# Kernel tuning notes

Measured on AMD Instinct MI355X. Metric: run time of the kernel, lower is better.

## Reference

```python
import jax, jax.numpy as jnp
import numpy as np
import math

NUM_HEADS = 16
THETA = 10000.0


def _rope(x):
    # x: (B, L, H, hd); interleaved-pair rotary embedding
    B, L, H, hd = x.shape
    inv_freq = 1.0 / (THETA ** (jnp.arange(0, hd, 2, dtype=jnp.float32) / hd))  # (hd/2,)
    ang = jnp.arange(L, dtype=jnp.float32)[:, None] * inv_freq[None, :]         # (L, hd/2)
    cos = jnp.cos(ang)[None, :, None, :].astype(x.dtype)
    sin = jnp.sin(ang)[None, :, None, :].astype(x.dtype)
    x1 = x[..., 0::2]
    x2 = x[..., 1::2]
    r1 = x1 * cos - x2 * sin
    r2 = x1 * sin + x2 * cos
    return jnp.stack([r1, r2], axis=-1).reshape(x.shape)


def setup_inputs() -> dict:
    key = jax.random.key(0)
    ks = jax.random.split(key, 5)
    B, L, D = 4, 2048, 1024
    x = jax.random.normal(ks[0], (B, L, D), dtype=jnp.float32)
    scale = 0.02
    wq = jax.random.normal(ks[1], (D, D), dtype=jnp.float32) * scale
    wk = jax.random.normal(ks[2], (D, D), dtype=jnp.float32) * scale
    wv = jax.random.normal(ks[3], (D, D), dtype=jnp.float32) * scale
    wo = jax.random.normal(ks[4], (D, D), dtype=jnp.float32) * scale
    return {"x": x, "wq": wq, "wk": wk, "wv": wv, "wo": wo}


def reference(x, wq, wk, wv, wo):
    B, L, D = x.shape
    H = NUM_HEADS
    hd = D // H
    q = (x @ wq).reshape(B, L, H, hd)
    k = (x @ wk).reshape(B, L, H, hd)
    v = (x @ wv).reshape(B, L, H, hd)
    q = _rope(q)
    k = _rope(k)
    # (B, H, L, hd)
    q = q.transpose(0, 2, 1, 3)
    k = k.transpose(0, 2, 1, 3)
    v = v.transpose(0, 2, 1, 3)
    # default-mask path of forward(): float 0/1 mask over key positions added to scores
    mask = (jnp.sum(x, axis=-1) != 0).astype(x.dtype)[:, None, None, :]  # (B,1,1,L)
    scale_factor = 1.0 / math.sqrt(hd)
    scores = jnp.einsum("bhld,bhsd->bhls", q, k) * scale_factor + mask
    attn = jax.nn.softmax(scores, axis=-1)
    out = jnp.einsum("bhls,bhsd->bhld", attn, v)          # (B,H,L,hd)
    out = out.transpose(0, 2, 1, 3).reshape(B, L, D)
    return out @ wo
```

## Files before the change

### kernel.cpp

```cpp
#include <hip/hip_runtime.h>

typedef __bf16 bf16_t;
typedef bf16_t bf16x8 __attribute__((ext_vector_type(8)));
typedef bf16_t bf16x4 __attribute__((ext_vector_type(4)));
typedef float f32x4 __attribute__((ext_vector_type(4)));

__device__ __forceinline__ ushort f2bu(float f) {
  unsigned u = __float_as_uint(f);
  unsigned r = (u + 0x7fffu + ((u >> 16) & 1u)) >> 16;
  return (ushort)r;
}
__device__ __forceinline__ float b2f(ushort u) {
  return __uint_as_float(((unsigned)u) << 16);
}

typedef const __attribute__((address_space(1))) unsigned int* gas_ptr;
typedef __attribute__((address_space(3))) unsigned int* las_ptr;
__device__ __forceinline__ void g2l16(const void* g, void* l) {
  __builtin_amdgcn_global_load_lds((gas_ptr)g, (las_ptr)l, 16, 0, 0);
}

__global__ __launch_bounds__(256) void pack_x(const float* __restrict__ x,
                                              ushort* __restrict__ xb,
                                              float* __restrict__ maskv) {
  int row = blockIdx.x;
  int tid = threadIdx.x;
  const float4 v = ((const float4*)(x + (size_t)row * 1024))[tid];
  ushort4 o;
  o.x = f2bu(v.x); o.y = f2bu(v.y); o.z = f2bu(v.z); o.w = f2bu(v.w);
  ((ushort4*)(xb + (size_t)row * 1024))[tid] = o;
  float s = v.x + v.y + v.z + v.w;
#pragma unroll
  for (int m = 1; m < 64; m <<= 1) s += __shfl_xor(s, m);
  __shared__ float wsum[4];
  if ((tid & 63) == 0) wsum[tid >> 6] = s;
  __syncthreads();
  if (tid == 0)
    maskv[row] = ((wsum[0] + wsum[1] + wsum[2] + wsum[3]) != 0.f)
                     ? 1.4426950408889634f : 0.f;
}

__global__ __launch_bounds__(1024) void pack_w(const float* __restrict__ w,
                                               ushort* __restrict__ wt) {
  __shared__ float t[32][33];
  int n0 = blockIdx.x * 32, k0 = blockIdx.y * 32;
  int tx = threadIdx.x, ty = threadIdx.y;
  t[ty][tx] = w[(size_t)(k0 + ty) * 1024 + n0 + tx];
  __syncthreads();
  wt[(size_t)(n0 + ty) * 1024 + k0 + tx] = f2bu(t[tx][ty]);
}

__global__ __launch_bounds__(256) void gemm_bf16(const ushort* __restrict__ A,
                                                 const ushort* __restrict__ BT,
                                                 void* __restrict__ Cv,
                                                 int M, int N, int K, int mode) {
  __shared__ ushort lA[128 * 64];
  __shared__ ushort lB[128 * 64];
  const int tid = threadIdx.x;
  const int wave = tid >> 6, lane = tid & 63;
  const int lr = lane & 15, lk = lane >> 4;
  const int bm = blockIdx.x * 128, bn = blockIdx.y * 128;
  const int wr = (wave >> 1) * 64, wc = (wave & 1) * 64;
  f32x4 acc[4][4] = {};
  for (int kt = 0; kt < K; kt += 64) {
#pragma unroll
    for (int t = 0; t < 4; ++t) {
      int e = (t * 256 + tid) * 8;
      int row = e >> 6, col = e & 63;
      g2l16(A + (size_t)(bm + row) * K + kt + col, lA + e);
      g2l16(BT + (size_t)(bn + row) * K + kt + col, lB + e);
    }
    __syncthreads();
#pragma unroll
    for (int ks = 0; ks < 2; ++ks) {
      bf16x8 af[4], bfr[4];
#pragma unroll
      for (int i = 0; i < 4; ++i)
        af[i] = *(const bf16x8*)(lA + (wr + i * 16 + lr) * 64 + ks * 32 + lk * 8);
#pragma unroll
      for (int j = 0; j < 4; ++j)
        bfr[j] = *(const bf16x8*)(lB + (wc + j * 16 + lr) * 64 + ks * 32 + lk * 8);
#pragma unroll
      for (int i = 0; i < 4; ++i)
#pragma unroll
        for (int j = 0; j < 4; ++j)
          acc[i][j] = __builtin_amdgcn_mfma_f32_16x16x32_bf16(af[i], bfr[j],
                                                              acc[i][j], 0, 0, 0);
    }
    __syncthreads();
  }
#pragma unroll
  for (int i = 0; i < 4; ++i)
#pragma unroll
    for (int j = 0; j < 4; ++j)
#pragma unroll
      for (int r = 0; r < 4; ++r) {
        int m = bm + wr + i * 16 + lk * 4 + r;
        int n = bn + wc + j * 16 + lr;
        float v = acc[i][j][r];
        if (mode == 2) {
          ((float*)Cv)[(size_t)m * N + n] = v;
        } else {
          int b = m >> 11, l = m & 2047;
          int h = n >> 6, d = n & 63;
          size_t addr;
          if (mode == 0) addr = (((size_t)b * 16 + h) * 2048 + l) * 64 + d;
          else           addr = (((size_t)b * 16 + h) * 64 + d) * 2048 + l;
          ((ushort*)Cv)[addr] = f2bu(v);
        }
      }
}

__global__ __launch_bounds__(256) void rope_k(ushort* __restrict__ Qb,
                                              ushort* __restrict__ Kb) {
  const size_t P1 = (size_t)64 * 2048 * 32;
  size_t id = (size_t)blockIdx.x * 256 + threadIdx.x;
  ushort* base = Qb;
  size_t rr = id;
  if (id >= P1) { base = Kb; rr = id - P1; }
  int i = (int)(rr & 31);
  int l = (int)((rr >> 5) & 2047);
  size_t bh = rr >> 16;
  size_t addr = (bh * 2048 + (size_t)l) * 64 + 2 * i;
  unsigned p = *(const unsigned*)(base + addr);
  float x1 = b2f((ushort)(p & 0xffffu));
  float x2 = b2f((ushort)(p >> 16));
  const float c = 0.41524101186092029f;
  float inv = exp2f(-c * (float)i);
  float ang = (float)l * inv;
  float sv, cv;
  sincosf(ang, &sv, &cv);
  float r1 = x1 * cv - x2 * sv;
  float r2 = x1 * sv + x2 * cv;
  unsigned o = (unsigned)f2bu(r1) | ((unsigned)f2bu(r2) << 16);
  *(unsigned*)(base + addr) = o;
}

__global__ __launch_bounds__(256) void attn_k(const ushort* __restrict__ Qb,
                                              const ushort* __restrict__ Kb,
                                              const ushort* __restrict__ VTb,
                                              const float* __restrict__ maskv,
                                              ushort* __restrict__ Ob) {
  __shared__ ushort lK[128 * 64];
  __shared__ ushort lV[64 * 128];
  __shared__ ushort lP[4][32 * 128];
  const int tid = threadIdx.x;
  const int wave = tid >> 6, lane = tid & 63;
  const int lr = lane & 15, lk = lane >> 4;
  const int bh = blockIdx.y;
  const int b = bh >> 4, h = bh & 15;
  const int q0 = blockIdx.x * 128 + wave * 32;
  const ushort* qp = Qb + (size_t)bh * 2048 * 64;
  const ushort* kp = Kb + (size_t)bh * 2048 * 64;
  const ushort* vp = VTb + (size_t)bh * 64 * 2048;
  const float SCL = 0.18033688011112042f;

  bf16x8 qfr[2][2];
#pragma unroll
  for (int qf = 0; qf < 2; ++qf)
#pragma unroll
    for (int ks = 0; ks < 2; ++ks)
      qfr[qf][ks] = *(const bf16x8*)(qp + (size_t)(q0 + qf * 16 + lr) * 64 +
                                     ks * 32 + lk * 8);

  float m2[2] = {-1e30f, -1e30f}, ls[2] = {0.f, 0.f};
  f32x4 oacc[2][4] = {};

  const int krow = tid >> 3;
  const int kslot = (tid & 7) ^ (krow & 7);
  const int vrow = tid >> 4;
  const int vslot = (tid & 15) ^ (vrow & 15);

  for (int kt = 0; kt < 16; ++kt) {
#pragma unroll
    for (int t = 0; t < 4; ++t) {
      g2l16(kp + (size_t)(kt * 128 + t * 32 + krow) * 64 + kslot * 8,
            lK + (t * 256 + tid) * 8);
      g2l16(vp + (size_t)(t * 16 + vrow) * 2048 + kt * 128 + vslot * 8,
            lV + (t * 256 + tid) * 8);
    }
    __syncthreads();

    f32x4 sacc[8][2] = {};
#pragma unroll
    for (int ks = 0; ks < 2; ++ks)
#pragma unroll
      for (int kf = 0; kf < 8; ++kf) {
        bf16x8 kfr = *(const bf16x8*)(lK + (kf * 16 + lr) * 64 +
                                      ((ks * 32 + lk * 8) ^ ((lr & 7) << 3)));
#pragma unroll
        for (int qf = 0; qf < 2; ++qf)
          sacc[kf][qf] = __builtin_amdgcn_mfma_f32_16x16x32_bf16(
              kfr, qfr[qf][ks], sacc[kf][qf], 0, 0, 0);
      }

    const f32x4* mrow = (const f32x4*)(maskv + (size_t)b * 2048 + kt * 128);
#pragma unroll
    for (int kf = 0; kf < 8; ++kf) {
      f32x4 mk = mrow[kf * 4 + lk];
#pragma unroll
      for (int qf = 0; qf < 2; ++qf) sacc[kf][qf] = sacc[kf][qf] * SCL + mk;
    }

    float corr[2];
#pragma unroll
    for (int qf = 0; qf < 2; ++qf) {
      float mx = -1e30f;
#pragma unroll
      for (int kf = 0; kf < 8; ++kf)
#pragma unroll
        for (int r = 0; r < 4; ++r) mx = fmaxf(mx, sacc[kf][qf][r]);
      mx = fmaxf(mx, __shfl_xor(mx, 16));
      mx = fmaxf(mx, __shfl_xor(mx, 32));
      float mnew = fmaxf(m2[qf], mx);
      corr[qf] = __builtin_amdgcn_exp2f(m2[qf] - mnew);
      m2[qf] = mnew;
      float ps = 0.f;
#pragma unroll
      for (int kf = 0; kf < 8; ++kf) {
        f32x4 p;
#pragma unroll
        for (int r = 0; r < 4; ++r)
          p[r] = __builtin_amdgcn_exp2f(sacc[kf][qf][r] - mnew);
        ps += (p[0] + p[1]) + (p[2] + p[3]);
        bf16x4 pb;
#pragma unroll
        for (int r = 0; r < 4; ++r) pb[r] = (bf16_t)p[r];
        int slot = (kf * 2 + (lk >> 1)) ^ lr;
        *(bf16x4*)&lP[wave][(qf * 16 + lr) * 128 + slot * 8 + (lk & 1) * 4] = pb;
      }
      ps += __shfl_xor(ps, 16);
      ps += __shfl_xor(ps, 32);
      ls[qf] = ls[qf] * corr[qf] + ps;
    }

#pragma unroll
    for (int mf = 0; mf < 2; ++mf)
#pragma unroll
      for (int r = 0; r < 4; ++r) {
        float c = __shfl(corr[mf], lk * 4 + r);
#pragma unroll
        for (int df = 0; df < 4; ++df) oacc[mf][df][r] *= c;
      }

#pragma unroll
    for (int ks2 = 0; ks2 < 4; ++ks2) {
      bf16x8 pf[2];
#pragma unroll
      for (int mf = 0; mf < 2; ++mf)
        pf[mf] = *(const bf16x8*)(&lP[wave][(mf * 16 + lr) * 128 +
                                            (((ks2 * 4 + lk) ^ lr) << 3)]);
#pragma unroll
      for (int df = 0; df < 4; ++df) {
        bf16x8 vf = *(const bf16x8*)(lV + (df * 16 + lr) * 128 +
                                     ((ks2 * 32 + lk * 8) ^ (lr << 3)));
#pragma unroll
        for (int mf = 0; mf < 2; ++mf)
          oacc[mf][df] = __builtin_amdgcn_mfma_f32_16x16x32_bf16(
              pf[mf], vf, oacc[mf][df], 0, 0, 0);
      }
    }
    __syncthreads();
  }

#pragma unroll
  for (int mf = 0; mf < 2; ++mf) {
    float inv[4];
#pragma unroll
    for (int r = 0; r < 4; ++r) inv[r] = 1.f / __shfl(ls[mf], lk * 4 + r);
#pragma unroll
    for (int df = 0; df < 4; ++df)
#pragma unroll
      for (int r = 0; r < 4; ++r) {
        int l = q0 + mf * 16 + lk * 4 + r;
        int d = df * 16 + lr;
        Ob[((size_t)b * 2048 + l) * 1024 + h * 64 + d] =
            f2bu(oacc[mf][df][r] * inv[r]);
      }
  }
}

extern "C" void kernel_launch(void* const* d_in, const int* in_sizes, int n_in,
                              void* d_out, int out_size, void* d_ws, size_t ws_size,
                              hipStream_t stream) {
  const float* x  = (const float*)d_in[0];
  const float* wq = (const float*)d_in[1];
  const float* wk = (const float*)d_in[2];
  const float* wv = (const float*)d_in[3];
  const float* wo = (const float*)d_in[4];
  float* out = (float*)d_out;
  char* ws = (char*)d_ws;
  const size_t MB = 1024 * 1024;
  ushort* xb   = (ushort*)(ws);
  ushort* ao   = (ushort*)(ws);
  ushort* wqT  = (ushort*)(ws + 16 * MB);
  ushort* wkT  = (ushort*)(ws + 18 * MB);
  ushort* wvT  = (ushort*)(ws + 20 * MB);
  ushort* woT  = (ushort*)(ws + 22 * MB);
  ushort* qb   = (ushort*)(ws + 24 * MB);
  ushort* kb   = (ushort*)(ws + 40 * MB);
  ushort* vtb  = (ushort*)(ws + 56 * MB);
  float* maskv = (float*)(ws + 72 * MB);

  pack_x<<<8192, 256, 0, stream>>>(x, xb, maskv);
  dim3 tb(32, 32);
  pack_w<<<dim3(32, 32), tb, 0, stream>>>(wq, wqT);
  pack_w<<<dim3(32, 32), tb, 0, stream>>>(wk, wkT);
  pack_w<<<dim3(32, 32), tb, 0, stream>>>(wv, wvT);
  pack_w<<<dim3(32, 32), tb, 0, stream>>>(wo, woT);
  gemm_bf16<<<dim3(64, 8), 256, 0, stream>>>(xb, wqT, qb, 8192, 1024, 1024, 0);
  gemm_bf16<<<dim3(64, 8), 256, 0, stream>>>(xb, wkT, kb, 8192, 1024, 1024, 0);
  gemm_bf16<<<dim3(64, 8), 256, 0, stream>>>(xb, wvT, vtb, 8192, 1024, 1024, 1);
  rope_k<<<32768, 256, 0, stream>>>(qb, kb);
  attn_k<<<dim3(16, 64), 256, 0, stream>>>(qb, kb, vtb, maskv, ao);
  gemm_bf16<<<dim3(64, 8), 256, 0, stream>>>(ao, woT, out, 8192, 1024, 1024, 2);
}
```

Measured before the change: 411.4 us.

## Rewrite attention with 32x32 MFMA, register-held P, and double-buffered K/V

```diff
diff --git a/kernel.cpp b/kernel.cpp
--- a/kernel.cpp
+++ b/kernel.cpp
@@ -3,7 +3,10 @@
 typedef __bf16 bf16_t;
 typedef bf16_t bf16x8 __attribute__((ext_vector_type(8)));
 typedef bf16_t bf16x4 __attribute__((ext_vector_type(4)));
+typedef bf16_t bf16x2 __attribute__((ext_vector_type(2)));
 typedef float f32x4 __attribute__((ext_vector_type(4)));
+typedef float f32x16 __attribute__((ext_vector_type(16)));
+typedef unsigned int uint32x4 __attribute__((ext_vector_type(4)));
 
 __device__ __forceinline__ ushort f2bu(float f) {
   unsigned u = __float_as_uint(f);
@@ -136,148 +139,146 @@
   *(unsigned*)(base + addr) = o;
 }
 
-__global__ __launch_bounds__(256) void attn_k(const ushort* __restrict__ Qb,
-                                              const ushort* __restrict__ Kb,
-                                              const ushort* __restrict__ VTb,
-                                              const float* __restrict__ maskv,
-                                              ushort* __restrict__ Ob) {
-  __shared__ ushort lK[128 * 64];
-  __shared__ ushort lV[64 * 128];
-  __shared__ ushort lP[4][32 * 128];
+__global__ __launch_bounds__(512, 4) void attn_k(const ushort* __restrict__ Qb,
+                                                 const ushort* __restrict__ Kb,
+                                                 const ushort* __restrict__ VTb,
+                                                 const float* __restrict__ maskv,
+                                                 ushort* __restrict__ Ob) {
+  __shared__ ushort lK[2][4096];
+  __shared__ ushort lV[2][4096];
   const int tid = threadIdx.x;
-  const int wave = tid >> 6, lane = tid & 63;
-  const int lr = lane & 15, lk = lane >> 4;
-  const int bh = blockIdx.y;
-  const int b = bh >> 4, h = bh & 15;
-  const int q0 = blockIdx.x * 128 + wave * 32;
+  const int wid = tid >> 6, lane = tid & 63;
+  const int q = lane & 31, hi = lane >> 5;
+  int f = blockIdx.x;
+  int swz = (f & 7) * 64 + (f >> 3);
+  int qb_i = swz & 7, bh = swz >> 3;
+  int b = bh >> 4, h = bh & 15;
+  const int q0w = qb_i * 256 + wid * 32;
   const ushort* qp = Qb + (size_t)bh * 2048 * 64;
   const ushort* kp = Kb + (size_t)bh * 2048 * 64;
   const ushort* vp = VTb + (size_t)bh * 64 * 2048;
   const float SCL = 0.18033688011112042f;
 
-  bf16x8 qfr[2][2];
-#pragma unroll
-  for (int qf = 0; qf < 2; ++qf)
-#pragma unroll
-    for (int ks = 0; ks < 2; ++ks)
-      qfr[qf][ks] = *(const bf16x8*)(qp + (size_t)(q0 + qf * 16 + lr) * 64 +
-                                     ks * 32 + lk * 8);
-
-  float m2[2] = {-1e30f, -1e30f}, ls[2] = {0.f, 0.f};
-  f32x4 oacc[2][4] = {};
-
-  const int krow = tid >> 3;
-  const int kslot = (tid & 7) ^ (krow & 7);
-  const int vrow = tid >> 4;
-  const int vslot = (tid & 15) ^ (vrow & 15);
-
-  for (int kt = 0; kt < 16; ++kt) {
-#pragma unroll
-    for (int t = 0; t < 4; ++t) {
-      g2l16(kp + (size_t)(kt * 128 + t * 32 + krow) * 64 + kslot * 8,
-            lK + (t * 256 + tid) * 8);
-      g2l16(vp + (size_t)(t * 16 + vrow) * 2048 + kt * 128 + vslot * 8,
-            lV + (t * 256 + tid) * 8);
+  bf16x8 qfr[4];
+#pragma unroll
+  for (int s = 0; s < 4; ++s)
+    qfr[s] = *(const bf16x8*)(qp + (size_t)(q0w + q) * 64 + s * 16 + hi * 8);
+
+  f32x16 oacc[2] = {};
+  float m2 = -1e30f, ls = 0.f;
+
+  const int sr = tid >> 3;
+  const int ss = (tid & 7) ^ (sr & 7);
+  const ushort* kg = kp + sr * 64 + ss * 8;
+  const ushort* vg = vp + (size_t)sr * 2048 + ss * 8;
+  int roff[4];
+#pragma unroll
+  for (int j = 0; j < 4; ++j)
+    roff[j] = q * 128 + (((2 * j + hi) ^ (q & 7)) << 4);
+
+  g2l16(kg, (char*)lK + tid * 16);
+  g2l16(vg, (char*)lV + tid * 16);
+  __syncthreads();
+
+  int cur = 0;
+  for (int kt = 0; kt < 32; ++kt) {
+    if (kt < 31) {
+      g2l16(kg + (kt + 1) * 4096, (char*)lK + (cur ^ 1) * 8192 + tid * 16);
+      g2l16(vg + (kt + 1) * 64,   (char*)lV + (cur ^ 1) * 8192 + tid * 16);
+    }
+    const char* bK = (const char*)lK + cur * 8192;
+    f32x16 sacc[2] = {};
+#pragma unroll
+    for (int kb2 = 0; kb2 < 2; ++kb2)
+#pragma unroll
+      for (int s = 0; s < 4; ++s) {
+        bf16x8 kfr = *(const bf16x8*)(bK + kb2 * 4096 + roff[s]);
+        sacc[kb2] = __builtin_amdgcn_mfma_f32_32x32x16_bf16(kfr, qfr[s],
+                                                            sacc[kb2], 0, 0, 0);
+      }
+    const float* mbase = maskv + (size_t)b * 2048 + kt * 64;
+#pragma unroll
+    for (int kb2 = 0; kb2 < 2; ++kb2)
+#pragma unroll
+      for (int g = 0; g < 4; ++g) {
+        f32x4 mv = *(const f32x4*)(mbase + kb2 * 32 + g * 8 + 4 * hi);
+#pragma unroll
+        for (int e = 0; e < 4; ++e)
+          sacc[kb2][4 * g + e] = sacc[kb2][4 * g + e] * SCL + mv[e];
+      }
+    float mx = -1e30f;
+#pragma unroll
+    for (int r = 0; r < 16; ++r) mx = fmaxf(mx, fmaxf(sacc[0][r], sacc[1][r]));
+    mx = fmaxf(mx, __shfl_xor(mx, 32));
+    float mnew = fmaxf(m2, mx);
+    float corr = __builtin_amdgcn_exp2f(m2 - mnew);
+    m2 = mnew;
+    float ps = 0.f;
+#pragma unroll
+    for (int kb2 = 0; kb2 < 2; ++kb2)
+#pragma unroll
+      for (int r = 0; r < 16; ++r) {
+        float p = __builtin_amdgcn_exp2f(sacc[kb2][r] - mnew);
+        sacc[kb2][r] = p;
+        ps += p;
+      }
+    ps += __shfl_xor(ps, 32);
+    ls = ls * corr + ps;
+#pragma unroll
+    for (int d2 = 0; d2 < 2; ++d2)
+#pragma unroll
+      for (int r = 0; r < 16; ++r) oacc[d2][r] *= corr;
+
+    const char* bV = (const char*)lV + cur * 8192;
+#pragma unroll
+    for (int kb2 = 0; kb2 < 2; ++kb2) {
+      unsigned w[8];
+#pragma unroll
+      for (int j = 0; j < 8; ++j) {
+        bf16x2 t2;
+        t2[0] = (bf16_t)sacc[kb2][2 * j];
+        t2[1] = (bf16_t)sacc[kb2][2 * j + 1];
+        w[j] = __builtin_bit_cast(unsigned, t2);
+      }
+#pragma unroll
+      for (int sg = 0; sg < 2; ++sg) {
+        unsigned X0 = (unsigned)__shfl_xor((int)w[4 * sg + 0], 32);
+        unsigned X1 = (unsigned)__shfl_xor((int)w[4 * sg + 1], 32);
+        unsigned X2 = (unsigned)__shfl_xor((int)w[4 * sg + 2], 32);
+        unsigned X3 = (unsigned)__shfl_xor((int)w[4 * sg + 3], 32);
+        uint32x4 fw;
+        fw[0] = hi ? X2 : w[4 * sg + 0];
+        fw[1] = hi ? X3 : w[4 * sg + 1];
+        fw[2] = hi ? w[4 * sg + 2] : X0;
+        fw[3] = hi ? w[4 * sg + 3] : X1;
+        bf16x8 pfr = __builtin_bit_cast(bf16x8, fw);
+        int tau = kb2 * 2 + sg;
+#pragma unroll
+        for (int d2 = 0; d2 < 2; ++d2) {
+          bf16x8 vfr = *(const bf16x8*)(bV + d2 * 4096 + roff[tau]);
+          oacc[d2] = __builtin_amdgcn_mfma_f32_32x32x16_bf16(vfr, pfr,
+                                                             oacc[d2], 0, 0, 0);
+        }
+      }
     }
     __syncthreads();
-
-    f32x4 sacc[8][2] = {};
-#pragma unroll
-    for (int ks = 0; ks < 2; ++ks)
-#pragma unroll
-      for (int kf = 0; kf < 8; ++kf) {
-        bf16x8 kfr = *(const bf16x8*)(lK + (kf * 16 + lr) * 64 +
-                                      ((ks * 32 + lk * 8) ^ ((lr & 7) << 3)));
-#pragma unroll
-        for (int qf = 0; qf < 2; ++qf)
-          sacc[kf][qf] = __builtin_amdgcn_mfma_f32_16x16x32_bf16(
-              kfr, qfr[qf][ks], sacc[kf][qf], 0, 0, 0);
-      }
-
-    const f32x4* mrow = (const f32x4*)(maskv + (size_t)b * 2048 + kt * 128);
-#pragma unroll
-    for (int kf = 0; kf < 8; ++kf) {
-      f32x4 mk = mrow[kf * 4 + lk];
-#pragma unroll
-      for (int qf = 0; qf < 2; ++qf) sacc[kf][qf] = sacc[kf][qf] * SCL + mk;
-    }
-
-    float corr[2];
-#pragma unroll
-    for (int qf = 0; qf < 2; ++qf) {
-      float mx = -1e30f;
-#pragma unroll
-      for (int kf = 0; kf < 8; ++kf)
-#pragma unroll
-        for (int r = 0; r < 4; ++r) mx = fmaxf(mx, sacc[kf][qf][r]);
-      mx = fmaxf(mx, __shfl_xor(mx, 16));
-      mx = fmaxf(mx, __shfl_xor(mx, 32));
-      float mnew = fmaxf(m2[qf], mx);
-      corr[qf] = __builtin_amdgcn_exp2f(m2[qf] - mnew);
-      m2[qf] = mnew;
-      float ps = 0.f;
-#pragma unroll
-      for (int kf = 0; kf < 8; ++kf) {
-        f32x4 p;
-#pragma unroll
-        for (int r = 0; r < 4; ++r)
-          p[r] = __builtin_amdgcn_exp2f(sacc[kf][qf][r] - mnew);
-        ps += (p[0] + p[1]) + (p[2] + p[3]);
-        bf16x4 pb;
-#pragma unroll
-        for (int r = 0; r < 4; ++r) pb[r] = (bf16_t)p[r];
-        int slot = (kf * 2 + (lk >> 1)) ^ lr;
-        *(bf16x4*)&lP[wave][(qf * 16 + lr) * 128 + slot * 8 + (lk & 1) * 4] = pb;
-      }
-      ps += __shfl_xor(ps, 16);
-      ps += __shfl_xor(ps, 32);
-      ls[qf] = ls[qf] * corr[qf] + ps;
-    }
-
-#pragma unroll
-    for (int mf = 0; mf < 2; ++mf)
-#pragma unroll
-      for (int r = 0; r < 4; ++r) {
-        float c = __shfl(corr[mf], lk * 4 + r);
-#pragma unroll
-        for (int df = 0; df < 4; ++df) oacc[mf][df][r] *= c;
-      }
-
-#pragma unroll
-    for (int ks2 = 0; ks2 < 4; ++ks2) {
-      bf16x8 pf[2];
-#pragma unroll
-      for (int mf = 0; mf < 2; ++mf)
-        pf[mf] = *(const bf16x8*)(&lP[wave][(mf * 16 + lr) * 128 +
-                                            (((ks2 * 4 + lk) ^ lr) << 3)]);
-#pragma unroll
-      for (int df = 0; df < 4; ++df) {
-        bf16x8 vf = *(const bf16x8*)(lV + (df * 16 + lr) * 128 +
-                                     ((ks2 * 32 + lk * 8) ^ (lr << 3)));
-#pragma unroll
-        for (int mf = 0; mf < 2; ++mf)
-          oacc[mf][df] = __builtin_amdgcn_mfma_f32_16x16x32_bf16(
-              pf[mf], vf, oacc[mf][df], 0, 0, 0);
-      }
-    }
-    __syncthreads();
+    cur ^= 1;
   }
 
-#pragma unroll
-  for (int mf = 0; mf < 2; ++mf) {
-    float inv[4];
-#pragma unroll
-    for (int r = 0; r < 4; ++r) inv[r] = 1.f / __shfl(ls[mf], lk * 4 + r);
-#pragma unroll
-    for (int df = 0; df < 4; ++df)
-#pragma unroll
-      for (int r = 0; r < 4; ++r) {
-        int l = q0 + mf * 16 + lk * 4 + r;
-        int d = df * 16 + lr;
-        Ob[((size_t)b * 2048 + l) * 1024 + h * 64 + d] =
-            f2bu(oacc[mf][df][r] * inv[r]);
-      }
-  }
+  float inv = 1.f / ls;
+  const int l = q0w + q;
+#pragma unroll
+  for (int d2 = 0; d2 < 2; ++d2)
+#pragma unroll
+    for (int g = 0; g < 4; ++g) {
+      ushort4 o;
+      o.x = f2bu(oacc[d2][4 * g + 0] * inv);
+      o.y = f2bu(oacc[d2][4 * g + 1] * inv);
+      o.z = f2bu(oacc[d2][4 * g + 2] * inv);
+      o.w = f2bu(oacc[d2][4 * g + 3] * inv);
+      int dcol = d2 * 32 + g * 8 + 4 * hi;
+      *(ushort4*)(Ob + ((size_t)b * 2048 + l) * 1024 + h * 64 + dcol) = o;
+    }
 }
 
 extern "C" void kernel_launch(void* const* d_in, const int* in_sizes, int n_in,
@@ -312,6 +313,6 @@
   gemm_bf16<<<dim3(64, 8), 256, 0, stream>>>(xb, wkT, kb, 8192, 1024, 1024, 0);
   gemm_bf16<<<dim3(64, 8), 256, 0, stream>>>(xb, wvT, vtb, 8192, 1024, 1024, 1);
   rope_k<<<32768, 256, 0, stream>>>(qb, kb);
-  attn_k<<<dim3(16, 64), 256, 0, stream>>>(qb, kb, vtb, maskv, ao);
+  attn_k<<<512, 512, 0, stream>>>(qb, kb, vtb, maskv, ao);
   gemm_bf16<<<dim3(64, 8), 256, 0, stream>>>(ao, woT, out, 8192, 1024, 1024, 2);
 }
```

Measured after the change: 353.7 us. -14.0%, faster.
